# Kernel tuning notes

Hardware: AMD Instinct MI355X
Metric: run time of the kernel (lower is better)

The kernel has to match this reference:

```python
import jax, jax.numpy as jnp
import numpy as np

H = 32          # num_heads
D = 64          # kv_channels (head dim)
HID = 2048      # hidden_size
MAXPOS = 2048   # max_seq_length


def _rotary_table(num_pos, dim):
    # [num_pos, dim]: sin for first dim/2 cols, cos for last dim/2 cols
    inv_freq = 1.0 / (10000.0 ** (jnp.arange(0, dim, 2, dtype=jnp.float32) / dim))
    t = jnp.arange(num_pos, dtype=jnp.float32)[:, None] * inv_freq[None, :]
    return jnp.concatenate([jnp.sin(t), jnp.cos(t)], axis=1)


def _apply_rope(x, sin, cos):
    # x: [B,S,H,D]; sin,cos: [B,S,D/2]
    sin = jnp.concatenate([sin, sin], axis=-1)[:, :, None, :]  # [B,S,1,D]
    cos = jnp.concatenate([cos, cos], axis=-1)[:, :, None, :]
    half = x.shape[-1] // 2
    x1, x2 = x[..., :half], x[..., half:]
    rot = jnp.concatenate([-x2, x1], axis=-1)
    return x * cos + rot * sin


def setup_inputs() -> dict:
    key = jax.random.key(0)
    k1, k2, k3, k4 = jax.random.split(key, 4)
    B, S = 2, 2048
    hidden_states = jax.random.normal(k1, (B, S, HID), jnp.float32)
    attention_mask = jax.random.randint(k2, (B, 1, S, S), 0, 2).astype(bool)
    position_ids = jnp.broadcast_to(jnp.arange(S, dtype=jnp.int32)[None, :], (B, S))
    W_qkv = jax.random.normal(k3, (3 * H * D, HID), jnp.float32) * 0.02
    W_o = jax.random.normal(k4, (HID, H * D), jnp.float32) * 0.02
    return {"hidden_states": hidden_states, "attention_mask": attention_mask,
            "position_ids": position_ids, "W_qkv": W_qkv, "W_o": W_o}


def reference(hidden_states, attention_mask, position_ids, W_qkv, W_o):
    B, S, _ = hidden_states.shape
    # fused QKV projection (nn.Linear: x @ W.T, no bias)
    qkv = hidden_states @ W_qkv.T                       # [B,S,3*H*D]
    qkv = qkv.reshape(B, S, H, 3 * D)
    q, k, v = jnp.split(qkv, 3, axis=-1)                # each [B,S,H,D]
    sincos = _rotary_table(MAXPOS, D)[position_ids]     # [B,S,D]
    sin, cos = jnp.split(sincos, 2, axis=-1)            # [B,S,D/2] each
    q = _apply_rope(q, sin, cos)
    k = _apply_rope(k, sin, cos)
    scale = jnp.sqrt(jnp.float32(D))
    scores = jnp.einsum('bqhd,bkhd->bhqk', q, k) / scale   # [B,H,S,S]
    scores = jnp.where(attention_mask, jnp.float32(-10000.0), scores)
    weights = jax.nn.softmax(scores, axis=-1)
    attn = jnp.einsum('bhqk,bkhd->bqhd', weights, v)       # [B,S,H,D]
    attn = attn.reshape(B, S, H * D)
    return attn @ W_o.T                                    # [B,S,HID]
```

## Files before the change

kernel.cpp:

```cpp
#include <hip/hip_runtime.h>

#define B_   2
#define S_   2048
#define H_   32
#define D_   64
#define HID_ 2048

typedef unsigned short ushort_t;
typedef __attribute__((ext_vector_type(8))) short short8;
typedef __attribute__((ext_vector_type(4))) float floatx4;

typedef const __attribute__((address_space(1))) char* gas_ptr;
typedef __attribute__((address_space(3))) char* las_ptr;

__device__ __forceinline__ float bf2f(ushort_t u) {
    union { unsigned int i; float f; } v; v.i = ((unsigned int)u) << 16; return v.f;
}
__device__ __forceinline__ ushort_t f2bf(float f) {
    union { float f; unsigned int i; } v; v.f = f;
    unsigned int x = v.i;
    unsigned int r = x + 0x7fffu + ((x >> 16) & 1u);
    return (ushort_t)(r >> 16);
}

__device__ __forceinline__ float fexp2(float x) {
#if __has_builtin(__builtin_amdgcn_exp2f)
    return __builtin_amdgcn_exp2f(x);
#else
    float r; asm("v_exp_f32 %0, %1" : "=v"(r) : "v"(x)); return r;
#endif
}

__device__ __forceinline__ unsigned cvt_pk_bf16(float a, float b) {
    unsigned r;
    asm("v_cvt_pk_bf16_f32 %0, %1, %2" : "=v"(r) : "v"(a), "v"(b));
    return r;
}

__global__ __launch_bounds__(256) void cast_f32_bf16(const float* __restrict__ in,
                                                     ushort_t* __restrict__ out,
                                                     int n8) {
    int i = blockIdx.x * 256 + threadIdx.x;
    if (i >= n8) return;
    const float4* p = (const float4*)(in + (size_t)i * 8);
    float4 a = p[0], b = p[1];
    uint4 o;
    o.x = cvt_pk_bf16(a.x, a.y);
    o.y = cvt_pk_bf16(a.z, a.w);
    o.z = cvt_pk_bf16(b.x, b.y);
    o.w = cvt_pk_bf16(b.z, b.w);
    *(uint4*)(out + (size_t)i * 8) = o;
}

__global__ __launch_bounds__(256) void mask_pack(const int* __restrict__ m,
                                                 unsigned long long* __restrict__ bits) {
    int idx = blockIdx.x * 256 + threadIdx.x;
    unsigned long long bal = __ballot(m[idx] != 0);
    if ((threadIdx.x & 63) == 0) bits[idx >> 6] = bal;
}

__global__ __launch_bounds__(512, 2) void gemm256_bt(const ushort_t* __restrict__ A,
                                                     const ushort_t* __restrict__ Bm,
                                                     ushort_t* __restrict__ C,
                                                     int M, int N, int K) {
    __shared__ ushort_t lA[2][256][64];
    __shared__ ushort_t lB[2][256][64];
    const int tid  = threadIdx.x;
    const int w    = tid >> 6, lane = tid & 63;
    const int quad = lane >> 4, l16 = lane & 15;
    const int wm = w >> 2, wn = w & 3;
    const int sr = lane >> 3, ss = lane & 7;
    const int gseg = (ss ^ sr) * 8;

    const int nbx = N >> 8;
    int id  = blockIdx.x;
    int cpx = gridDim.x >> 3;
    int swz = (id & 7) * cpx + (id >> 3);
    int by = swz / nbx, bx = swz - by * nbx;
    const int m0 = by * 256, n0 = bx * 256;

    int arow[2], brow[2];
    arow[0] = w * 8;                       arow[1] = 128 + w * 8;
    brow[0] = (w >> 2) * 64 + (w & 3) * 8; brow[1] = 128 + brow[0];

    const ushort_t *gAf[2], *gAs[2], *gBf[2], *gBs[2];
#pragma unroll
    for (int c = 0; c < 2; c++) {
        gAf[c] = A  + (size_t)(m0 + arow[c] + sr) * K + gseg;
        gAs[c] = A  + (size_t)(m0 + arow[c] + 64 + sr) * K + gseg;
        gBf[c] = Bm + (size_t)(n0 + brow[c] + sr) * K + gseg;
        gBs[c] = Bm + (size_t)(n0 + brow[c] + 32 + sr) * K + gseg;
    }

#define STAGE_AF(BUF, KT) do { _Pragma("unroll") for (int c = 0; c < 2; c++) \
    __builtin_amdgcn_global_load_lds((gas_ptr)(gAf[c] + (KT)), (las_ptr)&lA[BUF][arow[c]][0], 16, 0, 0); } while (0)
#define STAGE_AS(BUF, KT) do { _Pragma("unroll") for (int c = 0; c < 2; c++) \
    __builtin_amdgcn_global_load_lds((gas_ptr)(gAs[c] + (KT)), (las_ptr)&lA[BUF][arow[c] + 64][0], 16, 0, 0); } while (0)
#define STAGE_BF(BUF, KT) do { _Pragma("unroll") for (int c = 0; c < 2; c++) \
    __builtin_amdgcn_global_load_lds((gas_ptr)(gBf[c] + (KT)), (las_ptr)&lB[BUF][brow[c]][0], 16, 0, 0); } while (0)
#define STAGE_BS(BUF, KT) do { _Pragma("unroll") for (int c = 0; c < 2; c++) \
    __builtin_amdgcn_global_load_lds((gas_ptr)(gBs[c] + (KT)), (las_ptr)&lB[BUF][brow[c] + 32][0], 16, 0, 0); } while (0)

#define LDA_(SUB, BUF) do { _Pragma("unroll") for (int mi = 0; mi < 4; mi++) \
    _Pragma("unroll") for (int ks = 0; ks < 2; ks++) \
        aF[mi][ks] = *(const short8*)&lA[BUF][wm * 128 + (SUB) * 64 + mi * 16 + l16][(((ks * 4 + quad) ^ (l16 & 7)) * 8)]; } while (0)
#define LDB_(SUB, BUF) do { _Pragma("unroll") for (int ni = 0; ni < 2; ni++) \
    _Pragma("unroll") for (int ks = 0; ks < 2; ks++) \
        bF[ni][ks] = *(const short8*)&lB[BUF][wn * 64 + (SUB) * 32 + ni * 16 + l16][(((ks * 4 + quad) ^ (l16 & 7)) * 8)]; } while (0)

#define MM_(Hh, Gg) do { _Pragma("unroll") for (int mi = 0; mi < 4; mi++) \
    _Pragma("unroll") for (int ni = 0; ni < 2; ni++) \
    _Pragma("unroll") for (int ks = 0; ks < 2; ks++) \
        acc[(Hh) * 4 + mi][(Gg) * 2 + ni] = __builtin_amdgcn_mfma_f32_16x16x32_bf16( \
            aF[mi][ks], bF[ni][ks], acc[(Hh) * 4 + mi][(Gg) * 2 + ni], 0, 0, 0); } while (0)

#define VMC6 asm volatile("s_waitcnt vmcnt(6)" ::: "memory")
#define BARR __builtin_amdgcn_s_barrier()
#define SETP1 __builtin_amdgcn_s_setprio(1)
#define SETP0 __builtin_amdgcn_s_setprio(0)

    floatx4 acc[8][4];
#pragma unroll
    for (int i = 0; i < 8; i++)
#pragma unroll
        for (int j = 0; j < 4; j++) acc[i][j] = (floatx4){0.f, 0.f, 0.f, 0.f};
    short8 aF[4][2];
    short8 bF[2][2];

    const int NT = K >> 6;
    const int NI = NT >> 1;

    STAGE_AF(0, 0); STAGE_BF(0, 0); STAGE_AS(0, 0); STAGE_BS(0, 0);
    STAGE_BF(1, 64); STAGE_AS(1, 64); STAGE_BS(1, 64);
    VMC6;
    BARR;

    for (int i = 0; i < NI; ++i) {
        const int t1k = (i << 7) + 64;
        const int t2k = t1k + 64, t3k = t1k + 128;
        const bool g2 = (t2k < K), g3 = (t3k < K);
        const bool last = (i == NI - 1);

        LDA_(0, 0); LDB_(0, 0);
        STAGE_AF(1, t1k);
        asm volatile("s_waitcnt lgkmcnt(8)" ::: "memory");
        BARR; SETP1; MM_(0, 0); SETP0;
        VMC6; BARR;
        LDA_(1, 0);
        if (g2) STAGE_BF(0, t2k);
        BARR; SETP1; MM_(1, 0); SETP0;
        VMC6; BARR;
        LDB_(1, 0);
        if (g2) STAGE_AS(0, t2k);
        BARR; SETP1; MM_(1, 1); SETP0;
        VMC6; BARR;
        LDA_(0, 0);
        if (g2) STAGE_BS(0, t2k);
        BARR; SETP1; MM_(0, 1); SETP0;
        if (last) { asm volatile("s_waitcnt vmcnt(0)" ::: "memory"); }
        else      { VMC6; }
        BARR;

        LDA_(0, 1); LDB_(0, 1);
        if (g2) STAGE_AF(0, t2k);
        asm volatile("s_waitcnt lgkmcnt(8)" ::: "memory");
        BARR; SETP1; MM_(0, 0); SETP0;
        VMC6; BARR;
        LDA_(1, 1);
        if (g3) STAGE_BF(1, t3k);
        BARR; SETP1; MM_(1, 0); SETP0;
        VMC6; BARR;
        LDB_(1, 1);
        if (g3) STAGE_AS(1, t3k);
        BARR; SETP1; MM_(1, 1); SETP0;
        VMC6; BARR;
        LDA_(0, 1);
        if (g3) STAGE_BS(1, t3k);
        BARR; SETP1; MM_(0, 1); SETP0;
        VMC6; BARR;
    }

#pragma unroll
    for (int mi = 0; mi < 8; mi++)
#pragma unroll
        for (int ni = 0; ni < 4; ni++)
#pragma unroll
            for (int r = 0; r < 4; r++) {
                int row = m0 + wm * 128 + mi * 16 + quad * 4 + r;
                int col = n0 + wn * 64 + ni * 16 + l16;
                C[(size_t)row * N + col] = f2bf(acc[mi][ni][r]);
            }
#undef STAGE_AF
#undef STAGE_AS
#undef STAGE_BF
#undef STAGE_BS
#undef LDA_
#undef LDB_
#undef MM_
#undef VMC6
#undef BARR
#undef SETP1
#undef SETP0
}

template <bool OF32>
__global__ __launch_bounds__(512, 4) void gemm_wide_bt(const ushort_t* __restrict__ A,
                                                       const ushort_t* __restrict__ Bm,
                                                       void* __restrict__ Cv,
                                                       int M, int N, int K) {
    __shared__ ushort_t lA[128][32];
    __shared__ ushort_t lB[256][32];
    const int tid  = threadIdx.x;
    const int w    = tid >> 6, lane = tid & 63;
    const int quad = lane >> 4, l16 = lane & 15;
    const int wm = w >> 2, wn = w & 3;

    const int sr = lane >> 2, ss = lane & 3;
    const int gss = ss ^ ((sr >> 1) & 3);

    const int nbx = N >> 8;
    int id  = blockIdx.x;
    int cpx = gridDim.x >> 3;
    int swz = (id & 7) * cpx + (id >> 3);
    int by = swz / nbx, bx = swz - by * nbx;
    const int m0 = by * 128, n0 = bx * 256;

    const ushort_t* gA  = A  + (size_t)(m0 + w * 16 + sr) * K + gss * 8;
    const ushort_t* gB0 = Bm + (size_t)(n0 + w * 32 + sr) * K + gss * 8;
    const ushort_t* gB1 = gB0 + (size_t)16 * K;

    const int fseg = (quad ^ ((l16 >> 1) & 3)) * 8;

    floatx4 acc[4][4];
#pragma unroll
    for (int i = 0; i < 4; i++)
#pragma unroll
        for (int j = 0; j < 4; j++) acc[i][j] = (floatx4){0.f, 0.f, 0.f, 0.f};

    for (int k0 = 0; k0 < K; k0 += 32) {
        __builtin_amdgcn_global_load_lds((gas_ptr)(gA + k0),
                                         (las_ptr)&lA[w * 16][0], 16, 0, 0);
        __builtin_amdgcn_global_load_lds((gas_ptr)(gB0 + k0),
                                         (las_ptr)&lB[w * 32][0], 16, 0, 0);
        __builtin_amdgcn_global_load_lds((gas_ptr)(gB1 + k0),
                                         (las_ptr)&lB[w * 32 + 16][0], 16, 0, 0);
        __syncthreads();

        short8 aF[4], bF[4];
#pragma unroll
        for (int mi = 0; mi < 4; mi++)
            aF[mi] = *(const short8*)&lA[wm * 64 + mi * 16 + l16][fseg];
#pragma unroll
        for (int ni = 0; ni < 4; ni++)
            bF[ni] = *(const short8*)&lB[wn * 64 + ni * 16 + l16][fseg];
#pragma unroll
        for (int mi = 0; mi < 4; mi++)
#pragma unroll
            for (int ni = 0; ni < 4; ni++)
                acc[mi][ni] = __builtin_amdgcn_mfma_f32_16x16x32_bf16(aF[mi], bF[ni], acc[mi][ni], 0, 0, 0);
        __syncthreads();
    }

#pragma unroll
    for (int mi = 0; mi < 4; mi++)
#pragma unroll
        for (int ni = 0; ni < 4; ni++)
#pragma unroll
            for (int r = 0; r < 4; r++) {
                int row = m0 + wm * 64 + mi * 16 + quad * 4 + r;
                int col = n0 + wn * 64 + ni * 16 + l16;
                if (OF32) ((float*)Cv)[(size_t)row * N + col] = acc[mi][ni][r];
                else      ((ushort_t*)Cv)[(size_t)row * N + col] = f2bf(acc[mi][ni][r]);
            }
}

__global__ __launch_bounds__(256) void rope_qk(const ushort_t* __restrict__ qkv,
                                               const int* __restrict__ pos,
                                               ushort_t* __restrict__ qr,
                                               ushort_t* __restrict__ kr) {
    int idx = blockIdx.x * 256 + threadIdx.x;
    int d = idx & 63;
    int s = (idx >> 6) & 2047;
    int h = (idx >> 17) & 31;
    int b = idx >> 22;
    size_t qbase = ((size_t)(b * S_ + s)) * (3 * H_ * D_) + h * (3 * D_);
    int i  = d & 31;
    int d2 = d ^ 32;
    float x   = bf2f(qkv[qbase + d]);
    float xp  = bf2f(qkv[qbase + d2]);
    float kx  = bf2f(qkv[qbase + 64 + d]);
    float kxp = bf2f(qkv[qbase + 64 + d2]);
    int   p   = pos[b * S_ + s];
    float inv = fexp2((float)i * -0.41524101186092985f);
    float t   = (float)p * inv;
    float c = cosf(t), sn = sinf(t);
    float rq = (d < 32) ? -xp : xp;
    float rk = (d < 32) ? -kxp : kxp;
    float qo = (x * c + rq * sn) * 0.18033688011112042f;
    float ko = kx * c + rk * sn;
    size_t o = ((size_t)(b * H_ + h) * S_ + s) * D_ + d;
    qr[o] = f2bf(qo);
    kr[o] = f2bf(ko);
}

__global__ __launch_bounds__(256) void v_trans(const ushort_t* __restrict__ qkv,
                                               ushort_t* __restrict__ vt) {
    __shared__ ushort_t tile[64][72];
    const int bid = blockIdx.x;
    const int g  = bid >> 5;
    const int s0 = (bid & 31) * 64;
    const int b = g >> 5, h = g & 31;
    const int tid = threadIdx.x;
    const int r = tid >> 2, c = (tid & 3) * 16;
    const ushort_t* src = qkv + ((size_t)(b * S_) + s0 + r) * (3 * H_ * D_) + h * (3 * D_) + 128 + c;
    *(short8*)&tile[r][c]     = *(const short8*)src;
    *(short8*)&tile[r][c + 8] = *(const short8*)(src + 8);
    __syncthreads();
    const int d = tid >> 2, cs = (tid & 3) * 16;
    ushort_t* dst = vt + ((size_t)g * D_ + d) * S_ + s0 + cs;
    short8 o0, o1;
#pragma unroll
    for (int j = 0; j < 8; j++) {
        o0[j] = (short)tile[cs + j][d];
        o1[j] = (short)tile[cs + 8 + j][d];
    }
    *(short8*)dst       = o0;
    *(short8*)(dst + 8) = o1;
}

__global__ __launch_bounds__(256) void attn_kernel(const ushort_t* __restrict__ qr,
                                                   const ushort_t* __restrict__ kr,
                                                   const ushort_t* __restrict__ vt,
                                                   const unsigned long long* __restrict__ mbits,
                                                   ushort_t* __restrict__ ctx) {
    __shared__ ushort_t lK[64 * 64];
    __shared__ ushort_t lV[64 * 64];
    __shared__ ushort_t lds_p[4][16][72];
    const int tid  = threadIdx.x;
    const int wave = tid >> 6, lane = tid & 63;
    const int quad = lane >> 4, l16 = lane & 15;

    const int id   = blockIdx.x;
    const int g    = (id & 7) | ((id >> 8) << 3);
    const int qblk = (id >> 3) & 31;
    const int b    = g >> 5;
    const int q0   = qblk * 64 + wave * 16;
    const size_t headBase = (size_t)g * S_ * D_;
    const unsigned long long* mrow = mbits + ((size_t)b * S_ + q0 + l16) * (S_ / 64);

    const int sr = lane >> 3, ss = lane & 7;
    const int gss = ss ^ sr;
    const ushort_t* gK0 = kr + headBase + (size_t)(wave * 16 + sr) * D_ + gss * 8;
    const ushort_t* gV0 = vt + headBase + (size_t)(wave * 16 + sr) * S_ + gss * 8;

    const int segA0 = ((quad)     ^ (l16 & 7)) * 8;
    const int segA1 = ((quad + 4) ^ (l16 & 7)) * 8;
    const int rowOff = (l16)*64;

#define STAGE_T(K0) do { _Pragma("unroll") for (int i = 0; i < 2; i++) { \
    __builtin_amdgcn_global_load_lds((gas_ptr)(gK0 + (size_t)((K0) + i * 8) * D_), \
                                     (las_ptr)(lK + (wave * 16 + i * 8) * 64), 16, 0, 0); \
    __builtin_amdgcn_global_load_lds((gas_ptr)(gV0 + (size_t)(i * 8) * S_ + (K0)), \
                                     (las_ptr)(lV + (wave * 16 + i * 8) * 64), 16, 0, 0); } } while (0)

    short8 qf0 = *(const short8*)(qr + headBase + (size_t)(q0 + l16) * D_ + quad * 8);
    short8 qf1 = *(const short8*)(qr + headBase + (size_t)(q0 + l16) * D_ + 32 + quad * 8);

    float l_st = 0.f;
    floatx4 o[4];
#pragma unroll
    for (int t = 0; t < 4; t++) o[t] = (floatx4){0.f, 0.f, 0.f, 0.f};

    STAGE_T(0);

    for (int k0 = 0; k0 < S_; k0 += 64) {
        unsigned long long mb = mrow[k0 >> 6];
        __syncthreads();

        short8 kf[4][2], vf[4][2];
#pragma unroll
        for (int t = 0; t < 4; t++) {
            kf[t][0] = *(const short8*)&lK[t * 1024 + rowOff + segA0];
            kf[t][1] = *(const short8*)&lK[t * 1024 + rowOff + segA1];
            vf[t][0] = *(const short8*)&lV[t * 1024 + rowOff + segA0];
            vf[t][1] = *(const short8*)&lV[t * 1024 + rowOff + segA1];
        }
        __syncthreads();

        if (k0 + 64 < S_) STAGE_T(k0 + 64);

        floatx4 scT[4];
#pragma unroll
        for (int t = 0; t < 4; t++) scT[t] = (floatx4){0.f, 0.f, 0.f, 0.f};
#pragma unroll
        for (int t = 0; t < 4; t++) {
            scT[t] = __builtin_amdgcn_mfma_f32_16x16x32_bf16(kf[t][0], qf0, scT[t], 0, 0, 0);
            scT[t] = __builtin_amdgcn_mfma_f32_16x16x32_bf16(kf[t][1], qf1, scT[t], 0, 0, 0);
        }

        unsigned mlo = (unsigned)(mb >> (quad * 4));
        unsigned mhi = (unsigned)(mb >> (quad * 4 + 32));
        float pv[4][4];
        float rs = 0.f;
#pragma unroll
        for (int t = 0; t < 4; t++) {
            unsigned msrc = (t < 2) ? mlo : mhi;
#pragma unroll
            for (int r = 0; r < 4; r++) {
                int bitpos = (t & 1) * 16 + r;
                float e = fexp2(scT[t][r]);
                e = ((msrc >> bitpos) & 1u) ? 0.f : e;
                pv[t][r] = e;
                rs += e;
            }
        }
        l_st += rs;

#pragma unroll
        for (int t = 0; t < 4; t++) {
            uint2 w;
            w.x = cvt_pk_bf16(pv[t][0], pv[t][1]);
            w.y = cvt_pk_bf16(pv[t][2], pv[t][3]);
            *(uint2*)&lds_p[wave][l16][t * 16 + quad * 4] = w;
        }
        short8 pf0 = *(const short8*)&lds_p[wave][l16][quad * 8];
        short8 pf1 = *(const short8*)&lds_p[wave][l16][32 + quad * 8];

#pragma unroll
        for (int t = 0; t < 4; t++) {
            o[t] = __builtin_amdgcn_mfma_f32_16x16x32_bf16(pf0, vf[t][0], o[t], 0, 0, 0);
            o[t] = __builtin_amdgcn_mfma_f32_16x16x32_bf16(pf1, vf[t][1], o[t], 0, 0, 0);
        }
    }
#undef STAGE_T

    l_st += __shfl_xor(l_st, 16);
    l_st += __shfl_xor(l_st, 32);
    float li[4];
#pragma unroll
    for (int r = 0; r < 4; r++) li[r] = 1.0f / __shfl(l_st, quad * 4 + r, 16);
#pragma unroll
    for (int t = 0; t < 4; t++)
#pragma unroll
        for (int r = 0; r < 4; r++) {
            int srow = q0 + quad * 4 + r;
            ctx[((size_t)(b * S_) + srow) * (H_ * D_) + (g & 31) * D_ + t * 16 + l16] = f2bf(o[t][r] * li[r]);
        }
}

extern "C" void kernel_launch(void* const* d_in, const int* in_sizes, int n_in,
                              void* d_out, int out_size, void* d_ws, size_t ws_size,
                              hipStream_t stream) {
    const float* hidden          = (const float*)d_in[0];
    const int* mask              = (const int*)d_in[1];
    const int* pos               = (const int*)d_in[2];
    const float* Wqkv            = (const float*)d_in[3];
    const float* Wo              = (const float*)d_in[4];
    float* out                   = (float*)d_out;

    char* ws = (char*)d_ws;
    ushort_t* qkv     = (ushort_t*)(ws);
    ushort_t* ctx     = (ushort_t*)(ws);
    unsigned long long* mbits = (unsigned long long*)(ws + 16777216);
    ushort_t* Wo_bf   = (ushort_t*)(ws + 50331648);
    ushort_t* hid_bf  = (ushort_t*)(ws + 58720256);
    ushort_t* Wqkv_bf = (ushort_t*)(ws + 75497472);
    ushort_t* q_r     = (ushort_t*)(ws + 58720256);
    ushort_t* k_r     = (ushort_t*)(ws + 75497472);
    ushort_t* v_t     = (ushort_t*)(ws + 92274688);

    {
        int n8 = (B_ * S_ * HID_) / 8;
        cast_f32_bf16<<<n8 / 256, 256, 0, stream>>>(hidden, hid_bf, n8);
        n8 = (3 * H_ * D_ * HID_) / 8;
        cast_f32_bf16<<<n8 / 256, 256, 0, stream>>>(Wqkv, Wqkv_bf, n8);
        n8 = (HID_ * H_ * D_) / 8;
        cast_f32_bf16<<<n8 / 256, 256, 0, stream>>>(Wo, Wo_bf, n8);
    }

    gemm256_bt<<<((3 * H_ * D_) / 256) * ((B_ * S_) / 256), 512, 0, stream>>>(
        hid_bf, Wqkv_bf, qkv, B_ * S_, 3 * H_ * D_, HID_);

    int nElem = B_ * H_ * S_ * D_;
    rope_qk<<<nElem / 256, 256, 0, stream>>>(qkv, pos, q_r, k_r);
    v_trans<<<B_ * H_ * (S_ / 64), 256, 0, stream>>>(qkv, v_t);

    mask_pack<<<(B_ * S_ * S_) / 256, 256, 0, stream>>>(mask, mbits);

    attn_kernel<<<2048, 256, 0, stream>>>(q_r, k_r, v_t, mbits, ctx);

    gemm_wide_bt<true><<<(HID_ / 256) * ((B_ * S_) / 128), 512, 0, stream>>>(
        ctx, Wo_bf, out, B_ * S_, HID_, H_ * D_);
}
```

Baseline: 370.1 us.

## Merge cast launches, fuse RoPE into V transpose, raise MFMA wave priority

Merges the three f32-to-bf16 cast launches into one kernel that picks its source and destination by index range. Folds the RoPE kernel for Q and K into the V-transpose kernel, so one block handles 64 positions of one head and the separate launch is gone. Wraps the attention MFMA sections in s_setprio to favour waves issuing matrix ops. These save a few launches and some scheduling slack, but the fused RoPE loop has fewer blocks and more serial work per thread.

```diff
diff --git a/kernel.cpp b/kernel.cpp
--- a/kernel.cpp
+++ b/kernel.cpp
@@ -37,11 +37,15 @@
     return r;
 }
 
-__global__ __launch_bounds__(256) void cast_f32_bf16(const float* __restrict__ in,
-                                                     ushort_t* __restrict__ out,
-                                                     int n8) {
+__global__ __launch_bounds__(256) void cast3_f32_bf16(const float* __restrict__ in0, ushort_t* __restrict__ out0, int n0,
+                                                      const float* __restrict__ in1, ushort_t* __restrict__ out1, int n1,
+                                                      const float* __restrict__ in2, ushort_t* __restrict__ out2, int n2) {
     int i = blockIdx.x * 256 + threadIdx.x;
-    if (i >= n8) return;
+    const float* in; ushort_t* out;
+    if (i < n0)            { in = in0; out = out0; }
+    else if (i < n0 + n1)  { in = in1; out = out1; i -= n0; }
+    else if (i < n0 + n1 + n2) { in = in2; out = out2; i -= n0 + n1; }
+    else return;
     const float4* p = (const float4*)(in + (size_t)i * 8);
     float4 a = p[0], b = p[1];
     uint4 o;
@@ -274,36 +278,10 @@
             }
 }
 
-__global__ __launch_bounds__(256) void rope_qk(const ushort_t* __restrict__ qkv,
+__global__ __launch_bounds__(256) void rope_vt(const ushort_t* __restrict__ qkv,
                                                const int* __restrict__ pos,
                                                ushort_t* __restrict__ qr,
-                                               ushort_t* __restrict__ kr) {
-    int idx = blockIdx.x * 256 + threadIdx.x;
-    int d = idx & 63;
-    int s = (idx >> 6) & 2047;
-    int h = (idx >> 17) & 31;
-    int b = idx >> 22;
-    size_t qbase = ((size_t)(b * S_ + s)) * (3 * H_ * D_) + h * (3 * D_);
-    int i  = d & 31;
-    int d2 = d ^ 32;
-    float x   = bf2f(qkv[qbase + d]);
-    float xp  = bf2f(qkv[qbase + d2]);
-    float kx  = bf2f(qkv[qbase + 64 + d]);
-    float kxp = bf2f(qkv[qbase + 64 + d2]);
-    int   p   = pos[b * S_ + s];
-    float inv = fexp2((float)i * -0.41524101186092985f);
-    float t   = (float)p * inv;
-    float c = cosf(t), sn = sinf(t);
-    float rq = (d < 32) ? -xp : xp;
-    float rk = (d < 32) ? -kxp : kxp;
-    float qo = (x * c + rq * sn) * 0.18033688011112042f;
-    float ko = kx * c + rk * sn;
-    size_t o = ((size_t)(b * H_ + h) * S_ + s) * D_ + d;
-    qr[o] = f2bf(qo);
-    kr[o] = f2bf(ko);
-}
-
-__global__ __launch_bounds__(256) void v_trans(const ushort_t* __restrict__ qkv,
+                                               ushort_t* __restrict__ kr,
                                                ushort_t* __restrict__ vt) {
     __shared__ ushort_t tile[64][72];
     const int bid = blockIdx.x;
@@ -311,6 +289,35 @@
     const int s0 = (bid & 31) * 64;
     const int b = g >> 5, h = g & 31;
     const int tid = threadIdx.x;
+
+    {
+        const int d  = tid & 63;
+        const int r0 = tid >> 6;
+        const int i  = d & 31;
+        const int d2 = d ^ 32;
+        const float inv = fexp2((float)i * -0.41524101186092985f);
+        const ushort_t* qk0 = qkv + (size_t)(b * S_) * (3 * H_ * D_) + h * (3 * D_);
+#pragma unroll
+        for (int rr = 0; rr < 16; rr++) {
+            int s = s0 + r0 + rr * 4;
+            size_t qbase = (size_t)s * (3 * H_ * D_);
+            float x   = bf2f(qk0[qbase + d]);
+            float xp  = bf2f(qk0[qbase + d2]);
+            float kx  = bf2f(qk0[qbase + 64 + d]);
+            float kxp = bf2f(qk0[qbase + 64 + d2]);
+            int   p   = pos[b * S_ + s];
+            float t   = (float)p * inv;
+            float c = cosf(t), sn = sinf(t);
+            float rq = (d < 32) ? -xp : xp;
+            float rk = (d < 32) ? -kxp : kxp;
+            float qo = (x * c + rq * sn) * 0.18033688011112042f;
+            float ko = kx * c + rk * sn;
+            size_t o = ((size_t)g * S_ + s) * D_ + d;
+            qr[o] = f2bf(qo);
+            kr[o] = f2bf(ko);
+        }
+    }
+
     const int r = tid >> 2, c = (tid & 3) * 16;
     const ushort_t* src = qkv + ((size_t)(b * S_) + s0 + r) * (3 * H_ * D_) + h * (3 * D_) + 128 + c;
     *(short8*)&tile[r][c]     = *(const short8*)src;
@@ -392,11 +399,13 @@
         floatx4 scT[4];
 #pragma unroll
         for (int t = 0; t < 4; t++) scT[t] = (floatx4){0.f, 0.f, 0.f, 0.f};
+        __builtin_amdgcn_s_setprio(1);
 #pragma unroll
         for (int t = 0; t < 4; t++) {
             scT[t] = __builtin_amdgcn_mfma_f32_16x16x32_bf16(kf[t][0], qf0, scT[t], 0, 0, 0);
             scT[t] = __builtin_amdgcn_mfma_f32_16x16x32_bf16(kf[t][1], qf1, scT[t], 0, 0, 0);
         }
+        __builtin_amdgcn_s_setprio(0);
 
         unsigned mlo = (unsigned)(mb >> (quad * 4));
         unsigned mhi = (unsigned)(mb >> (quad * 4 + 32));
@@ -426,11 +435,13 @@
         short8 pf0 = *(const short8*)&lds_p[wave][l16][quad * 8];
         short8 pf1 = *(const short8*)&lds_p[wave][l16][32 + quad * 8];
 
+        __builtin_amdgcn_s_setprio(1);
 #pragma unroll
         for (int t = 0; t < 4; t++) {
             o[t] = __builtin_amdgcn_mfma_f32_16x16x32_bf16(pf0, vf[t][0], o[t], 0, 0, 0);
             o[t] = __builtin_amdgcn_mfma_f32_16x16x32_bf16(pf1, vf[t][1], o[t], 0, 0, 0);
         }
+        __builtin_amdgcn_s_setprio(0);
     }
 #undef STAGE_T
 
@@ -470,20 +481,19 @@
     ushort_t* v_t     = (ushort_t*)(ws + 92274688);
 
     {
-        int n8 = (B_ * S_ * HID_) / 8;
-        cast_f32_bf16<<<n8 / 256, 256, 0, stream>>>(hidden, hid_bf, n8);
-        n8 = (3 * H_ * D_ * HID_) / 8;
-        cast_f32_bf16<<<n8 / 256, 256, 0, stream>>>(Wqkv, Wqkv_bf, n8);
-        n8 = (HID_ * H_ * D_) / 8;
-        cast_f32_bf16<<<n8 / 256, 256, 0, stream>>>(Wo, Wo_bf, n8);
+        int n0 = (B_ * S_ * HID_) / 8;
+        int n1 = (3 * H_ * D_ * HID_) / 8;
+        int n2 = (HID_ * H_ * D_) / 8;
+        int nb = (n0 + n1 + n2 + 255) / 256;
+        cast3_f32_bf16<<<nb, 256, 0, stream>>>(hidden, hid_bf, n0,
+                                               Wqkv, Wqkv_bf, n1,
+                                               Wo, Wo_bf, n2);
     }
 
     gemm256_bt<<<((3 * H_ * D_) / 256) * ((B_ * S_) / 256), 512, 0, stream>>>(
         hid_bf, Wqkv_bf, qkv, B_ * S_, 3 * H_ * D_, HID_);
 
-    int nElem = B_ * H_ * S_ * D_;
-    rope_qk<<<nElem / 256, 256, 0, stream>>>(qkv, pos, q_r, k_r);
-    v_trans<<<B_ * H_ * (S_ / 64), 256, 0, stream>>>(qkv, v_t);
+    rope_vt<<<B_ * H_ * (S_ / 64), 256, 0, stream>>>(qkv, pos, q_r, k_r, v_t);
 
     mask_pack<<<(B_ * S_ * S_) / 256, 256, 0, stream>>>(mask, mbits);
 
```

After: 359.9 us. 1.03x faster.
